# Optimization experiments

Hardware: AMD Instinct MI355X
Metric: run time of the kernel (lower is better)

Reference implementation:

```python
import jax, jax.numpy as jnp
import numpy as np
import math

B, S, D, H = 2, 2048, 2048, 16
DH = D // H
SCALE = math.sqrt(DH)


def setup_inputs() -> dict:
    key = jax.random.key(0)
    ks = jax.random.split(key, 9)
    x = jax.random.normal(ks[0], (B, S, D), dtype=jnp.float32)
    # causal mask: True above the diagonal -> masked (matches masked_fill(mask, -inf))
    mask = jnp.triu(jnp.ones((S, S), dtype=jnp.bool_), k=1)
    std = 0.02
    wq = jax.random.normal(ks[1], (D, D), jnp.float32) * std
    wk = jax.random.normal(ks[2], (D, D), jnp.float32) * std
    wv = jax.random.normal(ks[3], (D, D), jnp.float32) * std
    wo = jax.random.normal(ks[4], (D, D), jnp.float32) * std
    bq = jnp.zeros((D,), jnp.float32)
    bk = jnp.zeros((D,), jnp.float32)
    bv = jnp.zeros((D,), jnp.float32)
    bo = jnp.zeros((D,), jnp.float32)
    return {"x": x, "mask": mask, "wq": wq, "bq": bq, "wk": wk, "bk": bk,
            "wv": wv, "bv": bv, "wo": wo, "bo": bo}


def reference(x, mask, wq, bq, wk, bk, wv, bv, wo, bo):
    b, s, d = x.shape
    # projections (nn.Linear: y = x @ W^T + b)
    q = (x @ wq.T + bq).reshape(b, s, H, DH).transpose(0, 2, 1, 3)  # [b,h,s,dh]
    k = (x @ wk.T + bk).reshape(b, s, H, DH).transpose(0, 2, 1, 3)
    v = (x @ wv.T + bv).reshape(b, s, H, DH).transpose(0, 2, 1, 3)
    scores = jnp.einsum('bhqd,bhkd->bhqk', q, k) / SCALE
    scores = jnp.where(mask[None, None, :, :], -jnp.inf, scores)
    attn = jax.nn.softmax(scores, axis=-1)
    out = jnp.einsum('bhqk,bhkd->bhqd', attn, v)  # [b,h,s,dh]
    out = out.transpose(0, 2, 1, 3).reshape(b, s, d)
    return out @ wo.T + bo
```

## Files before the change

kernel.cpp:

```cpp
#include <hip/hip_runtime.h>
#include <hip/hip_bf16.h>


using u16 = unsigned short;
typedef float  f32x4  __attribute__((ext_vector_type(4)));
typedef short  short8 __attribute__((ext_vector_type(8)));

#define DEV __device__ __forceinline__

constexpr int Bc = 2, Sc = 2048, Dc = 2048, Hc = 16, DHc = 128, Mc = 4096, Kc = 2048;
constexpr float RSCALE = 0.08838834764831845f;
constexpr float L2E    = 1.44269504088896341f;

DEV u16 f2bf(float f) { __bf16 h = (__bf16)f; return __builtin_bit_cast(u16, h); }

DEV void gload_lds16(const void* gsrc, void* lds) {
  __builtin_amdgcn_global_load_lds(
      (const __attribute__((address_space(1))) unsigned int*)gsrc,
      (__attribute__((address_space(3))) unsigned int*)lds, 16, 0, 0);
}

__global__ void cast_all(const float* __restrict__ x, const float* __restrict__ wq,
                         const float* __restrict__ wk, const float* __restrict__ wv,
                         const float* __restrict__ wo, u16* __restrict__ XB,
                         u16* __restrict__ WQKV, u16* __restrict__ WOb) {
  const int i = blockIdx.x * blockDim.x + threadIdx.x;
  const float4* src;
  u16* dst;
  if (i < 2097152)      { src = (const float4*)x  + i;             dst = XB   + (size_t)i * 4; }
  else if (i < 3145728) { src = (const float4*)wq + (i - 2097152); dst = WQKV + (size_t)(i - 2097152) * 4; }
  else if (i < 4194304) { src = (const float4*)wk + (i - 3145728); dst = WQKV + 4194304 + (size_t)(i - 3145728) * 4; }
  else if (i < 5242880) { src = (const float4*)wv + (i - 4194304); dst = WQKV + 8388608 + (size_t)(i - 4194304) * 4; }
  else                  { src = (const float4*)wo + (i - 5242880); dst = WOb  + (size_t)(i - 5242880) * 4; }
  float4 v = *src;
  u16 o0 = f2bf(v.x), o1 = f2bf(v.y), o2 = f2bf(v.z), o3 = f2bf(v.w);
  dst[0] = o0; dst[1] = o1; dst[2] = o2; dst[3] = o3;
}

template <int BM, int BN, int WM, int WN, int EPI>
__global__ __launch_bounds__(512, 2) void gemm2p(
    const u16* __restrict__ A, const u16* __restrict__ W,
    const float* __restrict__ bias0, const float* __restrict__ bias1,
    const float* __restrict__ bias2,
    u16* __restrict__ q_out, u16* __restrict__ k_out, u16* __restrict__ v_out,
    float* __restrict__ f_out) {
  constexpr int LA  = BM / 64;
  constexpr int LBH = BN / 128;
  constexpr int NH  = BN / 2;
  static_assert(LA + 2 * LBH == 6, "vmcnt immediates assume 6");
  constexpr int NWR = (EPI == 0) ? 6144 : 2048;
  constexpr int NBX = NWR / BN, NBY = Mc / BM, TOT = NBX * NBY, PX = TOT / 8;
  constexpr int NT = Kc / 64;

  __shared__ u16 lsA[2][BM * 64];
  __shared__ u16 lsB[2][BN * 64];

  const int tid = threadIdx.x;
  const int lane = tid & 63;
  const int w = tid >> 6;
  const int wr = w / WN, wc = w % WN;
  const int l15 = lane & 15, l4 = lane >> 4;

  const int id = blockIdx.x;
  const int wg = (id & 7) * PX + (id >> 3);
  const int bx = wg / NBY, by = wg % NBY;
  const int m0 = by * BM, n0 = bx * BN;

  const int srow = tid >> 3;
  const int spc = tid & 7;
  const int slc = spc ^ (srow & 7);

  auto stA = [&](int buf, int t, int j) {
    gload_lds16(A + (size_t)(m0 + j * 64 + srow) * Kc + t * 64 + slc * 8,
                &lsA[buf][j * 4096 + tid * 8]);
  };
  auto stB = [&](int buf, int t, int nq, int j) {
    const int wp = j * 64 + srow;
    const int n = (wp >> 5) * 64 + nq * 32 + (wp & 31);
    gload_lds16(W + (size_t)(n0 + n) * Kc + t * 64 + slc * 8,
                &lsB[buf][(nq * NH + j * 64) * 64 + tid * 8]);
  };

  const int pc0 = l4 ^ (l15 & 7);
  const int pc1 = (4 + l4) ^ (l15 & 7);

  f32x4 acc[4][4] = {};
  short8 af[8], b0[4], b1[4];

  auto ldA = [&](int buf) {
#pragma unroll
    for (int fm = 0; fm < 4; ++fm) {
      const u16* base = &lsA[buf][(wr * 64 + fm * 16 + l15) * 64];
      af[fm * 2 + 0] = *(const short8*)(base + pc0 * 8);
      af[fm * 2 + 1] = *(const short8*)(base + pc1 * 8);
    }
  };
  auto ldB = [&](int buf, int nq, short8* bf) {
#pragma unroll
    for (int f = 0; f < 2; ++f) {
      const u16* base = &lsB[buf][(nq * NH + wc * 32 + f * 16 + l15) * 64];
      bf[f * 2 + 0] = *(const short8*)(base + pc0 * 8);
      bf[f * 2 + 1] = *(const short8*)(base + pc1 * 8);
    }
  };
  auto mma = [&](const short8* bf, int nq) {
#pragma unroll
    for (int ks = 0; ks < 2; ++ks)
#pragma unroll
      for (int fm = 0; fm < 4; ++fm)
#pragma unroll
        for (int f = 0; f < 2; ++f)
          acc[fm][nq * 2 + f] = __builtin_amdgcn_mfma_f32_16x16x32_bf16(
              af[fm * 2 + ks], bf[f * 2 + ks], acc[fm][nq * 2 + f], 0, 0, 0);
  };

#pragma unroll
  for (int j = 0; j < LA; ++j) stA(0, 0, j);
#pragma unroll
  for (int j = 0; j < LBH; ++j) stB(0, 0, 0, j);
#pragma unroll
  for (int j = 0; j < LBH; ++j) stB(0, 0, 1, j);
#pragma unroll
  for (int j = 0; j < LA; ++j) stA(1, 1, j);
#pragma unroll
  for (int j = 0; j < LBH; ++j) stB(1, 1, 0, j);
  if constexpr (LA + LBH == 4) asm volatile("s_waitcnt vmcnt(4)" ::: "memory");
  else                         asm volatile("s_waitcnt vmcnt(5)" ::: "memory");
  __builtin_amdgcn_s_barrier();

#pragma unroll 1
  for (int u = 0; u < NT; ++u) {
    const int c = u & 1;
    ldA(c);
    ldB(c, 0, b0);
    if (u + 1 < NT) {
#pragma unroll
      for (int j = 0; j < LBH; ++j) stB(c ^ 1, u + 1, 1, j);
    }
    __builtin_amdgcn_s_barrier();
    asm volatile("s_waitcnt lgkmcnt(0)" ::: "memory");
    __builtin_amdgcn_s_setprio(1); mma(b0, 0); __builtin_amdgcn_s_setprio(0);
    if (u + 1 < NT) asm volatile("s_waitcnt vmcnt(6)" ::: "memory");
    else            asm volatile("s_waitcnt vmcnt(0)" ::: "memory");
    __builtin_amdgcn_s_barrier();
    ldB(c, 1, b1);
    if (u + 2 < NT) {
#pragma unroll
      for (int j = 0; j < LA; ++j) stA(c, u + 2, j);
#pragma unroll
      for (int j = 0; j < LBH; ++j) stB(c, u + 2, 0, j);
    }
    __builtin_amdgcn_s_barrier();
    asm volatile("s_waitcnt lgkmcnt(0)" ::: "memory");
    __builtin_amdgcn_s_setprio(1); mma(b1, 1); __builtin_amdgcn_s_setprio(0);
    if (u + 2 < NT) {
      asm volatile("s_waitcnt vmcnt(6)" ::: "memory");
    } else if (u + 1 < NT) {
      if constexpr (LBH == 2) asm volatile("s_waitcnt vmcnt(2)" ::: "memory");
      else                    asm volatile("s_waitcnt vmcnt(1)" ::: "memory");
    }
    __builtin_amdgcn_s_barrier();
  }

  if constexpr (EPI == 0) {
    const int sec = n0 >> 11;
    const int n0s = n0 & 2047;
    const float* bias = sec == 0 ? bias0 : (sec == 1 ? bias1 : bias2);
    u16* dst = sec == 0 ? q_out : (sec == 1 ? k_out : v_out);
    const float scl = sec == 0 ? RSCALE : 1.0f;
#pragma unroll
    for (int nf = 0; nf < 4; ++nf) {
      const int n2 = n0s + wc * 64 + nf * 16 + l15;
      const float bv_ = bias[n2];
      const int h = n2 >> 7, dh = n2 & 127;
#pragma unroll
      for (int fm = 0; fm < 4; ++fm)
#pragma unroll
        for (int r = 0; r < 4; ++r) {
          const int m = m0 + wr * 64 + fm * 16 + l4 * 4 + r;
          const int bb = m >> 11, s = m & 2047;
          dst[((size_t)(bb * Hc + h) * Sc + s) * DHc + dh] =
              f2bf((acc[fm][nf][r] + bv_) * scl);
        }
    }
  } else {
#pragma unroll
    for (int nf = 0; nf < 4; ++nf) {
      const int n = n0 + wc * 64 + nf * 16 + l15;
      const float bv_ = bias0[n];
#pragma unroll
      for (int fm = 0; fm < 4; ++fm)
#pragma unroll
        for (int r = 0; r < 4; ++r) {
          const int m = m0 + wr * 64 + fm * 16 + l4 * 4 + r;
          f_out[(size_t)m * Dc + n] = acc[fm][nf][r] + bv_;
        }
    }
  }
}

__global__ void transpose_v(const u16* __restrict__ V, u16* __restrict__ VT) {
  __shared__ u16 t[32][33];
  const int bh = blockIdx.z;
  const int s0 = blockIdx.x * 32;
  const int d0 = blockIdx.y * 32;
  const int tx = threadIdx.x, ty = threadIdx.y;
#pragma unroll
  for (int k = 0; k < 4; ++k)
    t[ty + 8 * k][tx] = V[((size_t)bh * Sc + s0 + ty + 8 * k) * DHc + d0 + tx];
  __syncthreads();
#pragma unroll
  for (int k = 0; k < 4; ++k)
    VT[((size_t)bh * DHc + d0 + ty + 8 * k) * Sc + s0 + tx] = t[tx][ty + 8 * k];
}

__global__ __launch_bounds__(256) void fattn(
    const u16* __restrict__ Qb, const u16* __restrict__ Kb,
    const u16* __restrict__ VTb, u16* __restrict__ AO) {
  __shared__ u16 lsK[2][64 * 128];
  __shared__ u16 lsV[2][128 * 64];
  __shared__ u16 lsP[4][16 * 64];

  const int tid = threadIdx.x;
  const int lane = tid & 63;
  const int w = tid >> 6;
  const int l15 = lane & 15, l4 = lane >> 4;

  const int id = blockIdx.x;
  const int xcd = id & 7, seq = id >> 3;
  const int bh = xcd + 8 * (seq >> 4);
  const int pair = seq & 15;

  const int b = bh >> 4, h = bh & 15;
  const size_t kbase = (size_t)bh * Sc * DHc;
  const size_t vbase = (size_t)bh * DHc * Sc;

#pragma unroll 1
  for (int qsel = 0; qsel < 2; ++qsel) {
    const int qt = qsel ? (31 - pair) : pair;
    const int q0 = qt * 64;
    const int ntiles = qt + 1;

    const size_t qbase = ((size_t)bh * Sc + q0 + w * 16 + l15) * DHc;
    short8 qf[4];
#pragma unroll
    for (int ks = 0; ks < 4; ++ks)
      qf[ks] = *(const short8*)&Qb[qbase + ks * 32 + l4 * 8];

    float m_run[4], l_run[4];
#pragma unroll
    for (int r = 0; r < 4; ++r) { m_run[r] = -__builtin_inff(); l_run[r] = 0.f; }
    f32x4 o_acc[8] = {};

    auto stageKV = [&](int sb, int ti) {
      const int kv0 = ti * 64;
#pragma unroll
      for (int c = 0; c < 4; ++c) {
        int p = c * 256 + tid;
        int row = p >> 4, ph = p & 15;
        int lg = (ph & 8) | ((ph ^ row) & 7);
        gload_lds16(Kb + kbase + (size_t)(kv0 + row) * DHc + lg * 8, &lsK[sb][p * 8]);
      }
#pragma unroll
      for (int c = 0; c < 4; ++c) {
        int p = c * 256 + tid;
        int row = p >> 3, ph = p & 7;
        int lg = ph ^ (row & 7);
        gload_lds16(VTb + vbase + (size_t)row * Sc + kv0 + lg * 8, &lsV[sb][p * 8]);
      }
    };

    stageKV(0, 0);
    asm volatile("s_waitcnt vmcnt(0)" ::: "memory");
    __syncthreads();

    int buf = 0;
#pragma unroll 1
    for (int ti = 0; ti < ntiles; ++ti) {
      const int kv0 = ti * 64;
      if (ti + 1 < ntiles) stageKV(buf ^ 1, ti + 1);

      f32x4 s[4] = {};
      __builtin_amdgcn_s_setprio(1);
#pragma unroll
      for (int nf = 0; nf < 4; ++nf) {
        int row = nf * 16 + l15;
#pragma unroll
        for (int ks = 0; ks < 4; ++ks) {
          int lg = ks * 4 + l4;
          int pc = (lg & 8) | ((lg ^ row) & 7);
          short8 kf = *(const short8*)&lsK[buf][row * 128 + pc * 8];
          s[nf] = __builtin_amdgcn_mfma_f32_16x16x32_bf16(qf[ks], kf, s[nf], 0, 0, 0);
        }
      }
      __builtin_amdgcn_s_setprio(0);

      if (kv0 == q0) {
#pragma unroll
        for (int nf = 0; nf < 4; ++nf) {
          int kc = nf * 16 + l15;
#pragma unroll
          for (int r = 0; r < 4; ++r)
            if (kc > w * 16 + l4 * 4 + r) s[nf][r] = -__builtin_inff();
        }
      }
      float alpha[4];
#pragma unroll
      for (int r = 0; r < 4; ++r) {
        float mx = fmaxf(fmaxf(s[0][r], s[1][r]), fmaxf(s[2][r], s[3][r]));
        mx = fmaxf(mx, __shfl_xor(mx, 1));
        mx = fmaxf(mx, __shfl_xor(mx, 2));
        mx = fmaxf(mx, __shfl_xor(mx, 4));
        mx = fmaxf(mx, __shfl_xor(mx, 8));
        float mnew = fmaxf(m_run[r], mx);
        alpha[r] = __builtin_amdgcn_exp2f((m_run[r] - mnew) * L2E);
        m_run[r] = mnew;
      }
#pragma unroll
      for (int nf = 0; nf < 4; ++nf)
#pragma unroll
        for (int r = 0; r < 4; ++r)
          s[nf][r] = __builtin_amdgcn_exp2f((s[nf][r] - m_run[r]) * L2E);
#pragma unroll
      for (int r = 0; r < 4; ++r) {
        float sm = s[0][r] + s[1][r] + s[2][r] + s[3][r];
        sm += __shfl_xor(sm, 1);
        sm += __shfl_xor(sm, 2);
        sm += __shfl_xor(sm, 4);
        sm += __shfl_xor(sm, 8);
        l_run[r] = l_run[r] * alpha[r] + sm;
      }
#pragma unroll
      for (int nf2 = 0; nf2 < 8; ++nf2)
#pragma unroll
        for (int r = 0; r < 4; ++r) o_acc[nf2][r] *= alpha[r];

#pragma unroll
      for (int nf = 0; nf < 4; ++nf)
#pragma unroll
        for (int r = 0; r < 4; ++r) {
          int rif = l4 * 4 + r;
          int kc = nf * 16 + l15;
          int pc = (kc >> 3) ^ (rif & 7);
          lsP[w][rif * 64 + pc * 8 + (kc & 7)] = f2bf(s[nf][r]);
        }
      asm volatile("s_waitcnt lgkmcnt(0)" ::: "memory");

      __builtin_amdgcn_s_setprio(1);
#pragma unroll
      for (int ks = 0; ks < 2; ++ks) {
        int pc = (ks * 4 + l4) ^ (l15 & 7);
        short8 pa = *(const short8*)&lsP[w][l15 * 64 + pc * 8];
#pragma unroll
        for (int nf2 = 0; nf2 < 8; ++nf2) {
          int vrow = nf2 * 16 + l15;
          int vpc = (ks * 4 + l4) ^ (vrow & 7);
          short8 vb = *(const short8*)&lsV[buf][vrow * 64 + vpc * 8];
          o_acc[nf2] = __builtin_amdgcn_mfma_f32_16x16x32_bf16(pa, vb, o_acc[nf2], 0, 0, 0);
        }
      }
      __builtin_amdgcn_s_setprio(0);

      asm volatile("s_waitcnt vmcnt(0)" ::: "memory");
      __syncthreads();
      buf ^= 1;
    }

#pragma unroll
    for (int nf2 = 0; nf2 < 8; ++nf2)
#pragma unroll
      for (int r = 0; r < 4; ++r) {
        int qr = q0 + w * 16 + l4 * 4 + r;
        float ov = o_acc[nf2][r] / l_run[r];
        AO[((size_t)(b * Sc + qr)) * Dc + h * DHc + nf2 * 16 + l15] = f2bf(ov);
      }
    __syncthreads();
  }
}

extern "C" void kernel_launch(void* const* d_in, const int* in_sizes, int n_in,
                              void* d_out, int out_size, void* d_ws, size_t ws_size,
                              hipStream_t stream) {
  const float* x  = (const float*)d_in[0];
  const float* wq = (const float*)d_in[2];
  const float* bq = (const float*)d_in[3];
  const float* wk = (const float*)d_in[4];
  const float* bk = (const float*)d_in[5];
  const float* wv = (const float*)d_in[6];
  const float* bv = (const float*)d_in[7];
  const float* wo = (const float*)d_in[8];
  const float* bo = (const float*)d_in[9];
  float* out = (float*)d_out;

  char* ws = (char*)d_ws;
  u16* WQKV = (u16*)(ws + 0);
  u16* WOb  = (u16*)(ws + 25165824);
  u16* XB   = (u16*)(ws + 33554432);
  u16* Qb   = (u16*)(ws + 50331648);
  u16* Kb   = (u16*)(ws + 67108864);
  u16* Vb   = (u16*)(ws + 83886080);
  u16* VTb  = (u16*)(ws + 100663296);
  u16* AO   = XB;

  cast_all<<<dim3(24576), dim3(256), 0, stream>>>(x, wq, wk, wv, wo, XB, WQKV, WOb);
  gemm2p<128, 256, 2, 4, 0><<<dim3(768), dim3(512), 0, stream>>>(
      XB, WQKV, bq, bk, bv, Qb, Kb, Vb, nullptr);
  transpose_v<<<dim3(64, 4, 32), dim3(32, 8), 0, stream>>>(Vb, VTb);
  fattn<<<dim3(512), dim3(256), 0, stream>>>(Qb, Kb, VTb, AO);
  gemm2p<256, 128, 4, 2, 1><<<dim3(256), dim3(512), 0, stream>>>(
      AO, WOb, bo, nullptr, nullptr, nullptr, nullptr, nullptr, out);
}
```

Measured before the change: 425.5 us.

## Fuse V transpose into QKV GEMM epilogue and retile GEMM to 256xBN

The QKV projection epilogue now writes V directly in transposed [b,h,dh,s] layout using packed 4-element stores, which removes the separate transpose_v kernel and the round trip of V through memory. The GEMM is retiled to a fixed 256-row M tile with a BN of 192 (QKV) or 128 (output), giving each wave 8xFR accumulators. The software pipeline is also restructured: B and half of A are prefetched before the first MMA half, and the other half of A before the second. The QKV launch drops from 768 to 512 blocks, which may change the wave count and occupancy relative to the CU count. The larger accumulator count adds register pressure.

```diff
diff --git a/kernel.cpp b/kernel.cpp
--- a/kernel.cpp
+++ b/kernel.cpp
@@ -37,34 +37,32 @@
   dst[0] = o0; dst[1] = o1; dst[2] = o2; dst[3] = o3;
 }
 
-template <int BM, int BN, int WM, int WN, int EPI>
+template <int BN, int FR, int EPI>
 __global__ __launch_bounds__(512, 2) void gemm2p(
     const u16* __restrict__ A, const u16* __restrict__ W,
     const float* __restrict__ bias0, const float* __restrict__ bias1,
     const float* __restrict__ bias2,
-    u16* __restrict__ q_out, u16* __restrict__ k_out, u16* __restrict__ v_out,
+    u16* __restrict__ q_out, u16* __restrict__ k_out, u16* __restrict__ vt_out,
     float* __restrict__ f_out) {
-  constexpr int LA  = BM / 64;
-  constexpr int LBH = BN / 128;
-  constexpr int NH  = BN / 2;
-  static_assert(LA + 2 * LBH == 6, "vmcnt immediates assume 6");
+  constexpr int LB = BN / 64;
   constexpr int NWR = (EPI == 0) ? 6144 : 2048;
-  constexpr int NBX = NWR / BN, NBY = Mc / BM, TOT = NBX * NBY, PX = TOT / 8;
+  constexpr int NBX = NWR / BN, NBY = Mc / 256, TOT = NBX * NBY, PX = TOT / 8;
   constexpr int NT = Kc / 64;
-
-  __shared__ u16 lsA[2][BM * 64];
+  static_assert(BN == FR * 64, "8 waves: 4 N-cols x 16*FR");
+
+  __shared__ u16 lsA[2][256 * 64];
   __shared__ u16 lsB[2][BN * 64];
 
   const int tid = threadIdx.x;
   const int lane = tid & 63;
   const int w = tid >> 6;
-  const int wr = w / WN, wc = w % WN;
+  const int wr = w >> 2, wc = w & 3;
   const int l15 = lane & 15, l4 = lane >> 4;
 
   const int id = blockIdx.x;
   const int wg = (id & 7) * PX + (id >> 3);
   const int bx = wg / NBY, by = wg % NBY;
-  const int m0 = by * BM, n0 = bx * BN;
+  const int m0 = by * 256, n0 = bx * BN;
 
   const int srow = tid >> 3;
   const int spc = tid & 7;
@@ -74,144 +72,123 @@
     gload_lds16(A + (size_t)(m0 + j * 64 + srow) * Kc + t * 64 + slc * 8,
                 &lsA[buf][j * 4096 + tid * 8]);
   };
-  auto stB = [&](int buf, int t, int nq, int j) {
-    const int wp = j * 64 + srow;
-    const int n = (wp >> 5) * 64 + nq * 32 + (wp & 31);
-    gload_lds16(W + (size_t)(n0 + n) * Kc + t * 64 + slc * 8,
-                &lsB[buf][(nq * NH + j * 64) * 64 + tid * 8]);
+  auto stB = [&](int buf, int t, int j) {
+    gload_lds16(W + (size_t)(n0 + j * 64 + srow) * Kc + t * 64 + slc * 8,
+                &lsB[buf][j * 4096 + tid * 8]);
   };
 
   const int pc0 = l4 ^ (l15 & 7);
   const int pc1 = (4 + l4) ^ (l15 & 7);
 
-  f32x4 acc[4][4] = {};
-  short8 af[8], b0[4], b1[4];
-
-  auto ldA = [&](int buf) {
+  f32x4 acc[8][FR] = {};
+  short8 af[8], bf[FR * 2];
+
+  auto ldA = [&](int buf, int half) {
 #pragma unroll
     for (int fm = 0; fm < 4; ++fm) {
-      const u16* base = &lsA[buf][(wr * 64 + fm * 16 + l15) * 64];
+      const u16* base = &lsA[buf][(wr * 128 + half * 64 + fm * 16 + l15) * 64];
       af[fm * 2 + 0] = *(const short8*)(base + pc0 * 8);
       af[fm * 2 + 1] = *(const short8*)(base + pc1 * 8);
     }
   };
-  auto ldB = [&](int buf, int nq, short8* bf) {
-#pragma unroll
-    for (int f = 0; f < 2; ++f) {
-      const u16* base = &lsB[buf][(nq * NH + wc * 32 + f * 16 + l15) * 64];
+  auto ldB = [&](int buf) {
+#pragma unroll
+    for (int f = 0; f < FR; ++f) {
+      const u16* base = &lsB[buf][(wc * (16 * FR) + f * 16 + l15) * 64];
       bf[f * 2 + 0] = *(const short8*)(base + pc0 * 8);
       bf[f * 2 + 1] = *(const short8*)(base + pc1 * 8);
     }
   };
-  auto mma = [&](const short8* bf, int nq) {
+  auto mma = [&](int half) {
 #pragma unroll
     for (int ks = 0; ks < 2; ++ks)
 #pragma unroll
       for (int fm = 0; fm < 4; ++fm)
 #pragma unroll
-        for (int f = 0; f < 2; ++f)
-          acc[fm][nq * 2 + f] = __builtin_amdgcn_mfma_f32_16x16x32_bf16(
-              af[fm * 2 + ks], bf[f * 2 + ks], acc[fm][nq * 2 + f], 0, 0, 0);
-  };
-
-#pragma unroll
-  for (int j = 0; j < LA; ++j) stA(0, 0, j);
-#pragma unroll
-  for (int j = 0; j < LBH; ++j) stB(0, 0, 0, j);
-#pragma unroll
-  for (int j = 0; j < LBH; ++j) stB(0, 0, 1, j);
-#pragma unroll
-  for (int j = 0; j < LA; ++j) stA(1, 1, j);
-#pragma unroll
-  for (int j = 0; j < LBH; ++j) stB(1, 1, 0, j);
-  if constexpr (LA + LBH == 4) asm volatile("s_waitcnt vmcnt(4)" ::: "memory");
-  else                         asm volatile("s_waitcnt vmcnt(5)" ::: "memory");
+        for (int f = 0; f < FR; ++f)
+          acc[half * 4 + fm][f] = __builtin_amdgcn_mfma_f32_16x16x32_bf16(
+              af[fm * 2 + ks], bf[f * 2 + ks], acc[half * 4 + fm][f], 0, 0, 0);
+  };
+
+#pragma unroll
+  for (int j = 0; j < LB; ++j) stB(0, 0, j);
+  stA(0, 0, 0); stA(0, 0, 2);
+  stA(0, 0, 1); stA(0, 0, 3);
+  asm volatile("s_waitcnt vmcnt(2)" ::: "memory");
   __builtin_amdgcn_s_barrier();
 
 #pragma unroll 1
   for (int u = 0; u < NT; ++u) {
     const int c = u & 1;
-    ldA(c);
-    ldB(c, 0, b0);
+    ldA(c, 0);
+    ldB(c);
     if (u + 1 < NT) {
 #pragma unroll
-      for (int j = 0; j < LBH; ++j) stB(c ^ 1, u + 1, 1, j);
+      for (int j = 0; j < LB; ++j) stB(c ^ 1, u + 1, j);
+      stA(c ^ 1, u + 1, 0); stA(c ^ 1, u + 1, 2);
     }
     __builtin_amdgcn_s_barrier();
     asm volatile("s_waitcnt lgkmcnt(0)" ::: "memory");
-    __builtin_amdgcn_s_setprio(1); mma(b0, 0); __builtin_amdgcn_s_setprio(0);
-    if (u + 1 < NT) asm volatile("s_waitcnt vmcnt(6)" ::: "memory");
-    else            asm volatile("s_waitcnt vmcnt(0)" ::: "memory");
+    __builtin_amdgcn_s_setprio(1); mma(0); __builtin_amdgcn_s_setprio(0);
+    if (u + 1 < NT) {
+      if constexpr (LB == 3) asm volatile("s_waitcnt vmcnt(5)" ::: "memory");
+      else                   asm volatile("s_waitcnt vmcnt(4)" ::: "memory");
+    } else {
+      asm volatile("s_waitcnt vmcnt(0)" ::: "memory");
+    }
     __builtin_amdgcn_s_barrier();
-    ldB(c, 1, b1);
-    if (u + 2 < NT) {
-#pragma unroll
-      for (int j = 0; j < LA; ++j) stA(c, u + 2, j);
-#pragma unroll
-      for (int j = 0; j < LBH; ++j) stB(c, u + 2, 0, j);
-    }
+    ldA(c, 1);
+    if (u + 1 < NT) { stA(c ^ 1, u + 1, 1); stA(c ^ 1, u + 1, 3); }
     __builtin_amdgcn_s_barrier();
     asm volatile("s_waitcnt lgkmcnt(0)" ::: "memory");
-    __builtin_amdgcn_s_setprio(1); mma(b1, 1); __builtin_amdgcn_s_setprio(0);
-    if (u + 2 < NT) {
-      asm volatile("s_waitcnt vmcnt(6)" ::: "memory");
-    } else if (u + 1 < NT) {
-      if constexpr (LBH == 2) asm volatile("s_waitcnt vmcnt(2)" ::: "memory");
-      else                    asm volatile("s_waitcnt vmcnt(1)" ::: "memory");
-    }
+    __builtin_amdgcn_s_setprio(1); mma(1); __builtin_amdgcn_s_setprio(0);
+    if (u + 1 < NT) asm volatile("s_waitcnt vmcnt(2)" ::: "memory");
     __builtin_amdgcn_s_barrier();
   }
 
   if constexpr (EPI == 0) {
-    const int sec = n0 >> 11;
-    const int n0s = n0 & 2047;
-    const float* bias = sec == 0 ? bias0 : (sec == 1 ? bias1 : bias2);
-    u16* dst = sec == 0 ? q_out : (sec == 1 ? k_out : v_out);
-    const float scl = sec == 0 ? RSCALE : 1.0f;
-#pragma unroll
-    for (int nf = 0; nf < 4; ++nf) {
-      const int n2 = n0s + wc * 64 + nf * 16 + l15;
-      const float bv_ = bias[n2];
+#pragma unroll
+    for (int f = 0; f < FR; ++f) {
+      const int n = n0 + wc * (16 * FR) + f * 16 + l15;
+      const int sec = n >> 11;
+      const int n2 = n & 2047;
+      const float bias = sec == 0 ? bias0[n2] : (sec == 1 ? bias1[n2] : bias2[n2]);
       const int h = n2 >> 7, dh = n2 & 127;
 #pragma unroll
-      for (int fm = 0; fm < 4; ++fm)
-#pragma unroll
-        for (int r = 0; r < 4; ++r) {
-          const int m = m0 + wr * 64 + fm * 16 + l4 * 4 + r;
-          const int bb = m >> 11, s = m & 2047;
-          dst[((size_t)(bb * Hc + h) * Sc + s) * DHc + dh] =
-              f2bf((acc[fm][nf][r] + bv_) * scl);
-        }
+      for (int fm = 0; fm < 8; ++fm) {
+        const int m = m0 + wr * 128 + fm * 16 + l4 * 4;
+        const int bb = m >> 11, s = m & 2047;
+        if (sec < 2) {
+          const float scl = sec == 0 ? RSCALE : 1.0f;
+          u16* dst = sec == 0 ? q_out : k_out;
+#pragma unroll
+          for (int r = 0; r < 4; ++r)
+            dst[((size_t)(bb * Hc + h) * Sc + s + r) * DHc + dh] =
+                f2bf((acc[fm][f][r] + bias) * scl);
+        } else {
+          ushort4 pk;
+          pk.x = f2bf(acc[fm][f][0] + bias);
+          pk.y = f2bf(acc[fm][f][1] + bias);
+          pk.z = f2bf(acc[fm][f][2] + bias);
+          pk.w = f2bf(acc[fm][f][3] + bias);
+          *(ushort4*)&vt_out[((size_t)(bb * Hc + h) * DHc + dh) * Sc + s] = pk;
+        }
+      }
     }
   } else {
 #pragma unroll
-    for (int nf = 0; nf < 4; ++nf) {
-      const int n = n0 + wc * 64 + nf * 16 + l15;
-      const float bv_ = bias0[n];
-#pragma unroll
-      for (int fm = 0; fm < 4; ++fm)
-#pragma unroll
-        for (int r = 0; r < 4; ++r) {
-          const int m = m0 + wr * 64 + fm * 16 + l4 * 4 + r;
-          f_out[(size_t)m * Dc + n] = acc[fm][nf][r] + bv_;
-        }
+    for (int f = 0; f < FR; ++f) {
+      const int n = n0 + wc * (16 * FR) + f * 16 + l15;
+      const float bias = bias0[n];
+#pragma unroll
+      for (int fm = 0; fm < 8; ++fm) {
+        const int m = m0 + wr * 128 + fm * 16 + l4 * 4;
+#pragma unroll
+        for (int r = 0; r < 4; ++r)
+          f_out[(size_t)(m + r) * Dc + n] = acc[fm][f][r] + bias;
+      }
     }
   }
-}
-
-__global__ void transpose_v(const u16* __restrict__ V, u16* __restrict__ VT) {
-  __shared__ u16 t[32][33];
-  const int bh = blockIdx.z;
-  const int s0 = blockIdx.x * 32;
-  const int d0 = blockIdx.y * 32;
-  const int tx = threadIdx.x, ty = threadIdx.y;
-#pragma unroll
-  for (int k = 0; k < 4; ++k)
-    t[ty + 8 * k][tx] = V[((size_t)bh * Sc + s0 + ty + 8 * k) * DHc + d0 + tx];
-  __syncthreads();
-#pragma unroll
-  for (int k = 0; k < 4; ++k)
-    VT[((size_t)bh * DHc + d0 + ty + 8 * k) * Sc + s0 + tx] = t[tx][ty + 8 * k];
 }
 
 __global__ __launch_bounds__(256) void fattn(
@@ -398,15 +375,13 @@
   u16* XB   = (u16*)(ws + 33554432);
   u16* Qb   = (u16*)(ws + 50331648);
   u16* Kb   = (u16*)(ws + 67108864);
-  u16* Vb   = (u16*)(ws + 83886080);
   u16* VTb  = (u16*)(ws + 100663296);
   u16* AO   = XB;
 
   cast_all<<<dim3(24576), dim3(256), 0, stream>>>(x, wq, wk, wv, wo, XB, WQKV, WOb);
-  gemm2p<128, 256, 2, 4, 0><<<dim3(768), dim3(512), 0, stream>>>(
-      XB, WQKV, bq, bk, bv, Qb, Kb, Vb, nullptr);
-  transpose_v<<<dim3(64, 4, 32), dim3(32, 8), 0, stream>>>(Vb, VTb);
+  gemm2p<192, 3, 0><<<dim3(512), dim3(512), 0, stream>>>(
+      XB, WQKV, bq, bk, bv, Qb, Kb, VTb, nullptr);
   fattn<<<dim3(512), dim3(256), 0, stream>>>(Qb, Kb, VTb, AO);
-  gemm2p<256, 128, 4, 2, 1><<<dim3(256), dim3(512), 0, stream>>>(
+  gemm2p<128, 2, 1><<<dim3(256), dim3(512), 0, stream>>>(
       AO, WOb, bo, nullptr, nullptr, nullptr, nullptr, nullptr, out);
 }
```

Measured after the change: 397.1 us. -6.7%, faster.
